# Performance work log

Measured on AMD Instinct MI355X. Metric: run time of the kernel, lower is better.

The kernel has to match this reference:

```python
import jax, jax.numpy as jnp
import numpy as np

N_NODES = 100000
N_EDGES = 1600000
N_GRAPHS = 64
IN_F = 128
H_F = 128
N_CLS = 10


def setup_inputs() -> dict:
    key = jax.random.key(0)
    ks = jax.random.split(key, 10)
    feat = jax.random.normal(ks[0], (N_NODES, IN_F), dtype=jnp.float32)
    W1 = jax.random.normal(ks[1], (IN_F, H_F), dtype=jnp.float32) * 0.05
    b1 = jax.random.normal(ks[2], (H_F,), dtype=jnp.float32) * 0.05
    W2 = jax.random.normal(ks[3], (H_F, H_F), dtype=jnp.float32) * 0.05
    b2 = jax.random.normal(ks[4], (H_F,), dtype=jnp.float32) * 0.05
    Wp = jax.random.normal(ks[5], (H_F, N_CLS), dtype=jnp.float32) * 0.05
    bp = jax.random.normal(ks[6], (N_CLS,), dtype=jnp.float32) * 0.05
    src = jax.random.randint(ks[7], (N_EDGES,), 0, N_NODES, dtype=jnp.int32)
    dst = jax.random.randint(ks[8], (N_EDGES,), 0, N_NODES, dtype=jnp.int32)
    graph_id = jnp.sort(jax.random.randint(ks[9], (N_NODES,), 0, N_GRAPHS, dtype=jnp.int32))
    return {"feat": feat, "W1": W1, "b1": b1, "W2": W2, "b2": b2,
            "Wp": Wp, "bp": bp, "src": src, "dst": dst, "graph_id": graph_id}


def reference(feat, W1, b1, W2, b2, Wp, bp, src, dst, graph_id):
    # copy_u + sum: each dst node sums features of its source neighbors
    def agg(h):
        return jax.ops.segment_sum(h[src], dst, num_segments=N_NODES)

    h = jax.nn.relu(agg(feat) @ W1 + b1)   # conv1 + ReLU
    h = jax.nn.relu(agg(h) @ W2 + b2)      # conv2 + ReLU (num_messagepasses=2)

    # dgl.mean_nodes: per-graph mean pooling over nodes
    sums = jax.ops.segment_sum(h, graph_id, num_segments=N_GRAPHS)      # [G, H]
    cnts = jax.ops.segment_sum(jnp.ones((N_NODES, 1), h.dtype), graph_id,
                               num_segments=N_GRAPHS)                    # [G, 1]
    graph_feats = sums / jnp.maximum(cnts, 1.0)
    return graph_feats @ Wp + bp
```

## Files before the change

kernel.cpp:

```cpp
#include <hip/hip_runtime.h>

#define NF 128
#define NGRAPHS 64
#define NCLS 10
#define NPARTS 256
#define PART_SHIFT 9
#define PART_NODES 512
#define PART_CAP 9216
#define SPLIT_TILE 4096
#define AS_STRIDE 136
#define SRC_BITS 17

typedef __attribute__((ext_vector_type(8))) short bf16x8;
typedef __attribute__((ext_vector_type(4))) float f32x4;
typedef __attribute__((ext_vector_type(8))) unsigned short u16x8;

__device__ __forceinline__ float bf2f(unsigned short u) {
    union { unsigned int i; float f; } v; v.i = ((unsigned int)u) << 16; return v.f;
}
__device__ __forceinline__ unsigned short f2bf(float f) {
    union { float f; unsigned int i; } v; v.f = f;
    unsigned int lsb = (v.i >> 16) & 1;
    v.i += 0x7fffu + lsb;
    return (unsigned short)(v.i >> 16);
}

__device__ __forceinline__ void gather_node(
    const unsigned short* __restrict__ x, const int* __restrict__ offs,
    const int* __restrict__ eid, int node, int n, int c, float acc[8]) {
#pragma unroll
    for (int r = 0; r < 8; ++r) acc[r] = 0.f;
    if (node >= n) return;
    int j = offs[node];
    int end = offs[node + 1];
    for (; j + 8 <= end; j += 8) {
        int s0 = eid[j + 0], s1 = eid[j + 1], s2 = eid[j + 2], s3 = eid[j + 3];
        int s4 = eid[j + 4], s5 = eid[j + 5], s6 = eid[j + 6], s7 = eid[j + 7];
        u16x8 v0 = ((const u16x8*)(x + (size_t)s0 * NF))[c];
        u16x8 v1 = ((const u16x8*)(x + (size_t)s1 * NF))[c];
        u16x8 v2 = ((const u16x8*)(x + (size_t)s2 * NF))[c];
        u16x8 v3 = ((const u16x8*)(x + (size_t)s3 * NF))[c];
        u16x8 v4 = ((const u16x8*)(x + (size_t)s4 * NF))[c];
        u16x8 v5 = ((const u16x8*)(x + (size_t)s5 * NF))[c];
        u16x8 v6 = ((const u16x8*)(x + (size_t)s6 * NF))[c];
        u16x8 v7 = ((const u16x8*)(x + (size_t)s7 * NF))[c];
#pragma unroll
        for (int r = 0; r < 8; ++r)
            acc[r] += ((bf2f(v0[r]) + bf2f(v1[r])) + (bf2f(v2[r]) + bf2f(v3[r])))
                    + ((bf2f(v4[r]) + bf2f(v5[r])) + (bf2f(v6[r]) + bf2f(v7[r])));
    }
    if (j + 4 <= end) {
        int s0 = eid[j + 0], s1 = eid[j + 1], s2 = eid[j + 2], s3 = eid[j + 3];
        u16x8 v0 = ((const u16x8*)(x + (size_t)s0 * NF))[c];
        u16x8 v1 = ((const u16x8*)(x + (size_t)s1 * NF))[c];
        u16x8 v2 = ((const u16x8*)(x + (size_t)s2 * NF))[c];
        u16x8 v3 = ((const u16x8*)(x + (size_t)s3 * NF))[c];
#pragma unroll
        for (int r = 0; r < 8; ++r)
            acc[r] += (bf2f(v0[r]) + bf2f(v1[r])) + (bf2f(v2[r]) + bf2f(v3[r]));
        j += 4;
    }
    for (; j < end; ++j) {
        int s0 = eid[j];
        u16x8 v0 = ((const u16x8*)(x + (size_t)s0 * NF))[c];
#pragma unroll
        for (int r = 0; r < 8; ++r) acc[r] += bf2f(v0[r]);
    }
}

__global__ __launch_bounds__(256) void split_prep_kernel(
    const int* __restrict__ src, const int* __restrict__ dst,
    unsigned int* __restrict__ records, int* __restrict__ gcur,
    const float* __restrict__ feat, unsigned short* __restrict__ featbf,
    const float* __restrict__ W1, const float* __restrict__ W2,
    unsigned short* __restrict__ Wt1, unsigned short* __restrict__ Wt2,
    float* __restrict__ sums, int ne, int nv4) {
    __shared__ unsigned int stage[SPLIT_TILE];
    __shared__ int hcnt[NPARTS];
    __shared__ int hscan[NPARTS];
    __shared__ int hcur[NPARTS];
    __shared__ int hg[NPARTS];
    int t = threadIdx.x;
    int gtid = blockIdx.x * 256 + t;
    int nthreads = gridDim.x * 256;

    for (int i = gtid; i < nv4; i += nthreads) {
        float4 v = ((const float4*)feat)[i];
        ushort4 o;
        o.x = f2bf(v.x); o.y = f2bf(v.y); o.z = f2bf(v.z); o.w = f2bf(v.w);
        ((ushort4*)featbf)[i] = o;
    }
    for (int i = gtid; i < 2 * NF * NF; i += nthreads) {
        const float* W = (i < NF * NF) ? W1 : W2;
        unsigned short* Wt = (i < NF * NF) ? Wt1 : Wt2;
        int id = i & (NF * NF - 1);
        int f = id >> 7;
        int k = id & 127;
        Wt[f * NF + k] = f2bf(W[k * NF + f]);
    }
    for (int i = gtid; i < NGRAPHS * NF; i += nthreads) sums[i] = 0.f;

    int tile0 = blockIdx.x * SPLIT_TILE;
    int cnt = min(SPLIT_TILE, ne - tile0);
    if (cnt <= 0) return;
    hcnt[t] = 0;
    __syncthreads();
    int dv[16], sv[16];
#pragma unroll
    for (int k2 = 0; k2 < 16; ++k2) {
        int i = k2 * 256 + t;
        if (i < cnt) {
            dv[k2] = dst[tile0 + i];
            sv[k2] = src[tile0 + i];
            atomicAdd(&hcnt[dv[k2] >> PART_SHIFT], 1);
        }
    }
    __syncthreads();
    hscan[t] = hcnt[t];
    __syncthreads();
    for (int off = 1; off < NPARTS; off <<= 1) {
        int v = (t >= off) ? hscan[t - off] : 0;
        __syncthreads();
        hscan[t] += v;
        __syncthreads();
    }
    hcur[t] = hscan[t] - hcnt[t];
    hg[t] = hcnt[t] ? atomicAdd(&gcur[t], hcnt[t]) : 0;
    __syncthreads();
#pragma unroll
    for (int k2 = 0; k2 < 16; ++k2) {
        int i = k2 * 256 + t;
        if (i < cnt) {
            int d = dv[k2];
            int pos = atomicAdd(&hcur[d >> PART_SHIFT], 1);
            stage[pos] = (((unsigned int)(d & (PART_NODES - 1))) << SRC_BITS)
                         | (unsigned int)sv[k2];
        }
    }
    __syncthreads();
    int grp = t >> 4;
    int lt = t & 15;
    for (int p = grp; p < NPARTS; p += 16) {
        int c = hcnt[p];
        if (c == 0) continue;
        int b = hscan[p] - c;
        int g = hg[p];
        if (g + c > PART_CAP) c = max(0, PART_CAP - g);
        unsigned int* outp = records + (size_t)p * PART_CAP + g;
        for (int i = lt; i < c; i += 16) outp[i] = stage[b + i];
    }
}

__global__ __launch_bounds__(256) void build_kernel(
    const unsigned int* __restrict__ records, const int* __restrict__ gcur,
    int* __restrict__ offs, int* __restrict__ eid, int n) {
    __shared__ int deg[PART_NODES];
    __shared__ int ps[NPARTS];
    __shared__ int wsum[4];
    __shared__ unsigned int rc[PART_CAP];
    int t = threadIdx.x;
    int p = blockIdx.x;

    ps[t] = min(gcur[t], PART_CAP);
    __syncthreads();
    for (int off = 1; off < NPARTS; off <<= 1) {
        int v = (t >= off) ? ps[t - off] : 0;
        __syncthreads();
        ps[t] += v;
        __syncthreads();
    }
    int L = min(gcur[p], PART_CAP);
    int base_g = ps[p] - L;
    if (p == 0 && t == 0) offs[n] = ps[NPARTS - 1];

    int lo = p << PART_SHIFT;
    int nn = min(n - lo, PART_NODES);
    if (nn <= 0) return;

    deg[t] = 0;
    deg[t + 256] = 0;
    __syncthreads();

    const unsigned int* rp = records + (size_t)p * PART_CAP;
    for (int i = t; i < L; i += 256) {
        unsigned int r = rp[i];
        rc[i] = r;
        atomicAdd(&deg[r >> SRC_BITS], 1);
    }
    __syncthreads();

    int v0 = deg[2 * t];
    int v1 = deg[2 * t + 1];
    int tsum = v0 + v1;
    int lane = t & 63, w = t >> 6;
    int sc = tsum;
    for (int off = 1; off < 64; off <<= 1) {
        int u = __shfl_up(sc, off, 64);
        if (lane >= off) sc += u;
    }
    if (lane == 63) wsum[w] = sc;
    __syncthreads();
    if (t == 0) {
        int a = 0;
        for (int k = 0; k < 4; ++k) { int v = wsum[k]; wsum[k] = a; a += v; }
    }
    __syncthreads();
    int run = sc - tsum + wsum[w];
    deg[2 * t] = run;
    if (2 * t < nn) offs[lo + 2 * t] = base_g + run;
    run += v0;
    deg[2 * t + 1] = run;
    if (2 * t + 1 < nn) offs[lo + 2 * t + 1] = base_g + run;
    __syncthreads();

    for (int i = t; i < L; i += 256) {
        unsigned int r = rc[i];
        int pos = atomicAdd(&deg[r >> SRC_BITS], 1);
        eid[base_g + pos] = (int)(r & ((1u << SRC_BITS) - 1));
    }
}

__global__ __launch_bounds__(256) void gather_gemm1(
    const unsigned short* __restrict__ x, const int* __restrict__ offs,
    const int* __restrict__ eid, const unsigned short* __restrict__ Wt,
    const float* __restrict__ bias, unsigned short* __restrict__ out, int n) {
    __shared__ unsigned short As[16 * AS_STRIDE];
    int wave = threadIdx.x >> 6;
    int lane = threadIdx.x & 63;
    int q = lane >> 4;
    int c = lane & 15;
    int node_base = blockIdx.x * 16;
    int row = wave * 4 + q;

    float acc[8];
    gather_node(x, offs, eid, node_base + row, n, c, acc);
    {
        u16x8 o;
#pragma unroll
        for (int r = 0; r < 8; ++r) o[r] = f2bf(acc[r]);
        *(u16x8*)(&As[row * AS_STRIDE + c * 8]) = o;
    }
    __syncthreads();

    int m16 = c;
    int n0 = wave * 32;
    const unsigned short* b0r = Wt + (size_t)(n0 + m16) * NF + q * 8;
    const unsigned short* b1r = b0r + 16 * NF;
    f32x4 acc0 = {0.f, 0.f, 0.f, 0.f};
    f32x4 acc1 = {0.f, 0.f, 0.f, 0.f};
#pragma unroll
    for (int kk = 0; kk < 4; ++kk) {
        bf16x8 a  = *(const bf16x8*)(&As[m16 * AS_STRIDE + kk * 32 + q * 8]);
        bf16x8 b0 = *(const bf16x8*)(b0r + kk * 32);
        bf16x8 b1 = *(const bf16x8*)(b1r + kk * 32);
        acc0 = __builtin_amdgcn_mfma_f32_16x16x32_bf16(a, b0, acc0, 0, 0, 0);
        acc1 = __builtin_amdgcn_mfma_f32_16x16x32_bf16(a, b1, acc1, 0, 0, 0);
    }
    float bias0 = bias[n0 + m16];
    float bias1 = bias[n0 + 16 + m16];
#pragma unroll
    for (int r = 0; r < 4; ++r) {
        int node = node_base + q * 4 + r;
        if (node >= n) break;
        unsigned short* o = out + (size_t)node * NF;
        o[n0 + m16]      = f2bf(fmaxf(acc0[r] + bias0, 0.f));
        o[n0 + 16 + m16] = f2bf(fmaxf(acc1[r] + bias1, 0.f));
    }
}

__global__ __launch_bounds__(256) void gather_gemm2_pool(
    const unsigned short* __restrict__ x, const int* __restrict__ offs,
    const int* __restrict__ eid, const unsigned short* __restrict__ Wt,
    const float* __restrict__ bias, const int* __restrict__ gid,
    float* __restrict__ sums, int n) {
    __shared__ unsigned short As[16 * AS_STRIDE];
    __shared__ float hblk[16][NF];
    int wave = threadIdx.x >> 6;
    int lane = threadIdx.x & 63;
    int q = lane >> 4;
    int c = lane & 15;
    int node_base = blockIdx.x * 16;
    int row = wave * 4 + q;

    float acc[8];
    gather_node(x, offs, eid, node_base + row, n, c, acc);
    {
        u16x8 o;
#pragma unroll
        for (int r = 0; r < 8; ++r) o[r] = f2bf(acc[r]);
        *(u16x8*)(&As[row * AS_STRIDE + c * 8]) = o;
    }
    __syncthreads();

    int m16 = c;
    int n0 = wave * 32;
    const unsigned short* b0r = Wt + (size_t)(n0 + m16) * NF + q * 8;
    const unsigned short* b1r = b0r + 16 * NF;
    f32x4 acc0 = {0.f, 0.f, 0.f, 0.f};
    f32x4 acc1 = {0.f, 0.f, 0.f, 0.f};
#pragma unroll
    for (int kk = 0; kk < 4; ++kk) {
        bf16x8 a  = *(const bf16x8*)(&As[m16 * AS_STRIDE + kk * 32 + q * 8]);
        bf16x8 b0 = *(const bf16x8*)(b0r + kk * 32);
        bf16x8 b1 = *(const bf16x8*)(b1r + kk * 32);
        acc0 = __builtin_amdgcn_mfma_f32_16x16x32_bf16(a, b0, acc0, 0, 0, 0);
        acc1 = __builtin_amdgcn_mfma_f32_16x16x32_bf16(a, b1, acc1, 0, 0, 0);
    }
    float bias0 = bias[n0 + m16];
    float bias1 = bias[n0 + 16 + m16];
#pragma unroll
    for (int r = 0; r < 4; ++r) {
        int rr = q * 4 + r;
        hblk[rr][n0 + m16]      = fmaxf(acc0[r] + bias0, 0.f);
        hblk[rr][n0 + 16 + m16] = fmaxf(acc1[r] + bias1, 0.f);
    }
    __syncthreads();

    int t = threadIdx.x;
    if (t < NF) {
        float accp = 0.f;
        int cur = -1;
        int lim = min(16, n - node_base);
        for (int i = 0; i < lim; ++i) {
            int g = gid[node_base + i];
            if (g != cur) {
                if (cur >= 0) atomicAdd(&sums[cur * NF + t], accp);
                accp = 0.f;
                cur = g;
            }
            accp += bf2f(f2bf(hblk[i][t]));
        }
        if (cur >= 0) atomicAdd(&sums[cur * NF + t], accp);
    }
}

__device__ __forceinline__ int lower_bound_i(const int* a, int n, int key) {
    int lo = 0, hi = n;
    while (lo < hi) {
        int mid = (lo + hi) >> 1;
        if (a[mid] < key) lo = mid + 1; else hi = mid;
    }
    return lo;
}

__global__ __launch_bounds__(64) void final_kernel(
    const float* __restrict__ sums, const int* __restrict__ gid, int n,
    const float* __restrict__ Wp, const float* __restrict__ bp,
    float* __restrict__ out) {
    __shared__ int range[2];
    int g = blockIdx.x;
    int c = threadIdx.x;
    if (c == 0) range[0] = lower_bound_i(gid, n, g);
    if (c == 1) range[1] = lower_bound_i(gid, n, g + 1);
    __syncthreads();
    if (c >= NCLS) return;
    float cnt = fmaxf((float)(range[1] - range[0]), 1.0f);
    float inv = 1.0f / cnt;
    float acc = bp[c];
#pragma unroll 8
    for (int k = 0; k < NF; ++k) {
        acc += sums[g * NF + k] * inv * Wp[k * NCLS + c];
    }
    out[g * NCLS + c] = acc;
}

extern "C" void kernel_launch(void* const* d_in, const int* in_sizes, int n_in,
                              void* d_out, int out_size, void* d_ws, size_t ws_size,
                              hipStream_t stream) {
    const float* feat = (const float*)d_in[0];
    const float* W1   = (const float*)d_in[1];
    const float* b1   = (const float*)d_in[2];
    const float* W2   = (const float*)d_in[3];
    const float* b2   = (const float*)d_in[4];
    const float* Wp   = (const float*)d_in[5];
    const float* bp   = (const float*)d_in[6];
    const int*   src  = (const int*)d_in[7];
    const int*   dst  = (const int*)d_in[8];
    const int*   gid  = (const int*)d_in[9];

    int ne = in_sizes[7];
    int n  = in_sizes[9];

    unsigned short* featbf = (unsigned short*)d_ws;
    unsigned short* h1     = featbf + (size_t)n * NF;
    unsigned int* records = (unsigned int*)(h1 + (size_t)n * NF);
    int* eid      = (int*)(records + (size_t)NPARTS * PART_CAP);
    float* sums   = (float*)(eid + ne);
    int* gcur     = (int*)(sums + NGRAPHS * NF);
    unsigned short* Wt1 = (unsigned short*)(gcur + NPARTS);
    unsigned short* Wt2 = Wt1 + NF * NF;
    int* offs     = (int*)(Wt2 + NF * NF);

    int nv4 = n * NF / 4;
    int splitblocks = (ne + SPLIT_TILE - 1) / SPLIT_TILE;
    int buildblocks = (n + PART_NODES - 1) >> PART_SHIFT;
    int ggblocks = (n + 15) / 16;

    hipMemsetAsync(gcur, 0, NPARTS * sizeof(int), stream);
    split_prep_kernel<<<splitblocks, 256, 0, stream>>>(
        src, dst, records, gcur, feat, featbf, W1, W2, Wt1, Wt2, sums, ne, nv4);
    build_kernel<<<buildblocks, 256, 0, stream>>>(records, gcur, offs, eid, n);

    gather_gemm1<<<ggblocks, 256, 0, stream>>>(featbf, offs, eid, Wt1, b1, h1, n);
    gather_gemm2_pool<<<ggblocks, 256, 0, stream>>>(h1, offs, eid, Wt2, b2, gid, sums, n);
    final_kernel<<<NGRAPHS, 64, 0, stream>>>(sums, gid, n, Wp, bp, (float*)d_out);
}
```

Baseline: 306.8 us.

## Slice features into 16-column planes and split gather from GEMM kernels

```diff
diff --git a/kernel.cpp b/kernel.cpp
--- a/kernel.cpp
+++ b/kernel.cpp
@@ -11,6 +11,10 @@
 #define AS_STRIDE 136
 #define SRC_BITS 17
 
+#define NSLICE 8
+#define SL 16
+#define AGG_TILE 32
+
 typedef __attribute__((ext_vector_type(8))) short bf16x8;
 typedef __attribute__((ext_vector_type(4))) float f32x4;
 typedef __attribute__((ext_vector_type(8))) unsigned short u16x8;
@@ -23,49 +27,6 @@
     unsigned int lsb = (v.i >> 16) & 1;
     v.i += 0x7fffu + lsb;
     return (unsigned short)(v.i >> 16);
-}
-
-__device__ __forceinline__ void gather_node(
-    const unsigned short* __restrict__ x, const int* __restrict__ offs,
-    const int* __restrict__ eid, int node, int n, int c, float acc[8]) {
-#pragma unroll
-    for (int r = 0; r < 8; ++r) acc[r] = 0.f;
-    if (node >= n) return;
-    int j = offs[node];
-    int end = offs[node + 1];
-    for (; j + 8 <= end; j += 8) {
-        int s0 = eid[j + 0], s1 = eid[j + 1], s2 = eid[j + 2], s3 = eid[j + 3];
-        int s4 = eid[j + 4], s5 = eid[j + 5], s6 = eid[j + 6], s7 = eid[j + 7];
-        u16x8 v0 = ((const u16x8*)(x + (size_t)s0 * NF))[c];
-        u16x8 v1 = ((const u16x8*)(x + (size_t)s1 * NF))[c];
-        u16x8 v2 = ((const u16x8*)(x + (size_t)s2 * NF))[c];
-        u16x8 v3 = ((const u16x8*)(x + (size_t)s3 * NF))[c];
-        u16x8 v4 = ((const u16x8*)(x + (size_t)s4 * NF))[c];
-        u16x8 v5 = ((const u16x8*)(x + (size_t)s5 * NF))[c];
-        u16x8 v6 = ((const u16x8*)(x + (size_t)s6 * NF))[c];
-        u16x8 v7 = ((const u16x8*)(x + (size_t)s7 * NF))[c];
-#pragma unroll
-        for (int r = 0; r < 8; ++r)
-            acc[r] += ((bf2f(v0[r]) + bf2f(v1[r])) + (bf2f(v2[r]) + bf2f(v3[r])))
-                    + ((bf2f(v4[r]) + bf2f(v5[r])) + (bf2f(v6[r]) + bf2f(v7[r])));
-    }
-    if (j + 4 <= end) {
-        int s0 = eid[j + 0], s1 = eid[j + 1], s2 = eid[j + 2], s3 = eid[j + 3];
-        u16x8 v0 = ((const u16x8*)(x + (size_t)s0 * NF))[c];
-        u16x8 v1 = ((const u16x8*)(x + (size_t)s1 * NF))[c];
-        u16x8 v2 = ((const u16x8*)(x + (size_t)s2 * NF))[c];
-        u16x8 v3 = ((const u16x8*)(x + (size_t)s3 * NF))[c];
-#pragma unroll
-        for (int r = 0; r < 8; ++r)
-            acc[r] += (bf2f(v0[r]) + bf2f(v1[r])) + (bf2f(v2[r]) + bf2f(v3[r]));
-        j += 4;
-    }
-    for (; j < end; ++j) {
-        int s0 = eid[j];
-        u16x8 v0 = ((const u16x8*)(x + (size_t)s0 * NF))[c];
-#pragma unroll
-        for (int r = 0; r < 8; ++r) acc[r] += bf2f(v0[r]);
-    }
 }
 
 __global__ __launch_bounds__(256) void split_prep_kernel(
@@ -83,12 +44,17 @@
     int t = threadIdx.x;
     int gtid = blockIdx.x * 256 + t;
     int nthreads = gridDim.x * 256;
+    int n_nodes = nv4 >> 5;
 
     for (int i = gtid; i < nv4; i += nthreads) {
         float4 v = ((const float4*)feat)[i];
         ushort4 o;
         o.x = f2bf(v.x); o.y = f2bf(v.y); o.z = f2bf(v.z); o.w = f2bf(v.w);
-        ((ushort4*)featbf)[i] = o;
+        int node = i >> 5;
+        int q4 = i & 31;
+        int s = q4 >> 2;
+        int cc = (q4 & 3) * 4;
+        *(ushort4*)(featbf + ((size_t)s * n_nodes + node) * SL + cc) = o;
     }
     for (int i = gtid; i < 2 * NF * NF; i += nthreads) {
         const float* W = (i < NF * NF) ? W1 : W2;
@@ -220,29 +186,86 @@
     }
 }
 
-__global__ __launch_bounds__(256) void gather_gemm1(
-    const unsigned short* __restrict__ x, const int* __restrict__ offs,
-    const int* __restrict__ eid, const unsigned short* __restrict__ Wt,
-    const float* __restrict__ bias, unsigned short* __restrict__ out, int n) {
+__global__ __launch_bounds__(256) void agg_slice(
+    const unsigned short* __restrict__ xs,
+    const int* __restrict__ offs, const int* __restrict__ eid,
+    unsigned short* __restrict__ out,
+    int n) {
+    __shared__ unsigned short ob[AGG_TILE * SL];
+    int b = blockIdx.x;
+    int s = b & 7;
+    int node0 = (b >> 3) * AGG_TILE;
+    const unsigned short* xb = xs + (size_t)s * n * SL;
+    int t = threadIdx.x;
+    int wave = t >> 6;
+    int lane = t & 63;
+    int hw = lane >> 5;
+    int l = lane & 31;
+    int slot = l >> 1;
+    int half = l & 1;
+
+#pragma unroll
+    for (int r = 0; r < AGG_TILE / 8; ++r) {
+        int node = node0 + r * 8 + wave * 2 + hw;
+        float acc[8] = {0.f, 0.f, 0.f, 0.f, 0.f, 0.f, 0.f, 0.f};
+        if (node < n) {
+            int beg = __builtin_nontemporal_load(offs + node);
+            int end = __builtin_nontemporal_load(offs + node + 1);
+            for (int j = beg + slot; j < end; j += 16) {
+                int srcv = __builtin_nontemporal_load(eid + j);
+                u16x8 v = *(const u16x8*)(xb + (size_t)srcv * SL + half * 8);
+#pragma unroll
+                for (int k = 0; k < 8; ++k) acc[k] += bf2f(v[k]);
+            }
+        }
+#pragma unroll
+        for (int m = 2; m <= 16; m <<= 1) {
+#pragma unroll
+            for (int k = 0; k < 8; ++k) acc[k] += __shfl_xor(acc[k], m, 64);
+        }
+        if (slot == 0) {
+            u16x8 o;
+#pragma unroll
+            for (int k = 0; k < 8; ++k) o[k] = f2bf(acc[k]);
+            *(u16x8*)(&ob[(r * 8 + wave * 2 + hw) * SL + half * 8]) = o;
+        }
+    }
+    __syncthreads();
+    int nrem = n - node0;
+    if (nrem > AGG_TILE) nrem = AGG_TILE;
+    if (nrem > 0) {
+        int cu16 = nrem * SL;
+        int i = t * 2;
+        if (i < cu16) {
+            unsigned int w = *(const unsigned int*)(&ob[i]);
+            *(unsigned int*)(out + ((size_t)s * n + node0) * SL + i) = w;
+        }
+    }
+}
+
+__global__ __launch_bounds__(256) void gemm_h1(
+    unsigned short* __restrict__ buf,
+    const unsigned short* __restrict__ Wt, const float* __restrict__ bias,
+    int n) {
     __shared__ unsigned short As[16 * AS_STRIDE];
-    int wave = threadIdx.x >> 6;
-    int lane = threadIdx.x & 63;
+    int t = threadIdx.x;
+    int node_base = blockIdx.x * 16;
+    {
+        int s = t >> 5;
+        int u = t & 31;
+        int r = u >> 1;
+        int hc = (u & 1) * 8;
+        int node = node_base + r;
+        u16x8 v = {0, 0, 0, 0, 0, 0, 0, 0};
+        if (node < n) v = *(const u16x8*)(buf + ((size_t)s * n + node) * SL + hc);
+        *(u16x8*)(&As[r * AS_STRIDE + s * SL + hc]) = v;
+    }
+    __syncthreads();
+
+    int wave = t >> 6;
+    int lane = t & 63;
     int q = lane >> 4;
-    int c = lane & 15;
-    int node_base = blockIdx.x * 16;
-    int row = wave * 4 + q;
-
-    float acc[8];
-    gather_node(x, offs, eid, node_base + row, n, c, acc);
-    {
-        u16x8 o;
-#pragma unroll
-        for (int r = 0; r < 8; ++r) o[r] = f2bf(acc[r]);
-        *(u16x8*)(&As[row * AS_STRIDE + c * 8]) = o;
-    }
-    __syncthreads();
-
-    int m16 = c;
+    int m16 = lane & 15;
     int n0 = wave * 32;
     const unsigned short* b0r = Wt + (size_t)(n0 + m16) * NF + q * 8;
     const unsigned short* b1r = b0r + 16 * NF;
@@ -262,37 +285,37 @@
     for (int r = 0; r < 4; ++r) {
         int node = node_base + q * 4 + r;
         if (node >= n) break;
-        unsigned short* o = out + (size_t)node * NF;
-        o[n0 + m16]      = f2bf(fmaxf(acc0[r] + bias0, 0.f));
-        o[n0 + 16 + m16] = f2bf(fmaxf(acc1[r] + bias1, 0.f));
-    }
-}
-
-__global__ __launch_bounds__(256) void gather_gemm2_pool(
-    const unsigned short* __restrict__ x, const int* __restrict__ offs,
-    const int* __restrict__ eid, const unsigned short* __restrict__ Wt,
-    const float* __restrict__ bias, const int* __restrict__ gid,
-    float* __restrict__ sums, int n) {
+        buf[((size_t)(2 * wave) * n + node) * SL + m16] =
+            f2bf(fmaxf(acc0[r] + bias0, 0.f));
+        buf[((size_t)(2 * wave + 1) * n + node) * SL + m16] =
+            f2bf(fmaxf(acc1[r] + bias1, 0.f));
+    }
+}
+
+__global__ __launch_bounds__(256) void gemm_h2_pool(
+    const unsigned short* __restrict__ buf,
+    const unsigned short* __restrict__ Wt, const float* __restrict__ bias,
+    const int* __restrict__ gid, float* __restrict__ sums, int n) {
     __shared__ unsigned short As[16 * AS_STRIDE];
     __shared__ float hblk[16][NF];
-    int wave = threadIdx.x >> 6;
-    int lane = threadIdx.x & 63;
+    int t = threadIdx.x;
+    int node_base = blockIdx.x * 16;
+    {
+        int s = t >> 5;
+        int u = t & 31;
+        int r = u >> 1;
+        int hc = (u & 1) * 8;
+        int node = node_base + r;
+        u16x8 v = {0, 0, 0, 0, 0, 0, 0, 0};
+        if (node < n) v = *(const u16x8*)(buf + ((size_t)s * n + node) * SL + hc);
+        *(u16x8*)(&As[r * AS_STRIDE + s * SL + hc]) = v;
+    }
+    __syncthreads();
+
+    int wave = t >> 6;
+    int lane = t & 63;
     int q = lane >> 4;
-    int c = lane & 15;
-    int node_base = blockIdx.x * 16;
-    int row = wave * 4 + q;
-
-    float acc[8];
-    gather_node(x, offs, eid, node_base + row, n, c, acc);
-    {
-        u16x8 o;
-#pragma unroll
-        for (int r = 0; r < 8; ++r) o[r] = f2bf(acc[r]);
-        *(u16x8*)(&As[row * AS_STRIDE + c * 8]) = o;
-    }
-    __syncthreads();
-
-    int m16 = c;
+    int m16 = lane & 15;
     int n0 = wave * 32;
     const unsigned short* b0r = Wt + (size_t)(n0 + m16) * NF + q * 8;
     const unsigned short* b1r = b0r + 16 * NF;
@@ -310,13 +333,12 @@
     float bias1 = bias[n0 + 16 + m16];
 #pragma unroll
     for (int r = 0; r < 4; ++r) {
-        int rr = q * 4 + r;
-        hblk[rr][n0 + m16]      = fmaxf(acc0[r] + bias0, 0.f);
-        hblk[rr][n0 + 16 + m16] = fmaxf(acc1[r] + bias1, 0.f);
-    }
-    __syncthreads();
-
-    int t = threadIdx.x;
+        int row = q * 4 + r;
+        hblk[row][n0 + m16]      = fmaxf(acc0[r] + bias0, 0.f);
+        hblk[row][n0 + 16 + m16] = fmaxf(acc1[r] + bias1, 0.f);
+    }
+    __syncthreads();
+
     if (t < NF) {
         float accp = 0.f;
         int cur = -1;
@@ -381,9 +403,9 @@
     int ne = in_sizes[7];
     int n  = in_sizes[9];
 
-    unsigned short* featbf = (unsigned short*)d_ws;
-    unsigned short* h1     = featbf + (size_t)n * NF;
-    unsigned int* records = (unsigned int*)(h1 + (size_t)n * NF);
+    unsigned short* bufA = (unsigned short*)d_ws;
+    unsigned short* bufB = bufA + (size_t)n * NF;
+    unsigned int* records = (unsigned int*)(bufB + (size_t)n * NF);
     int* eid      = (int*)(records + (size_t)NPARTS * PART_CAP);
     float* sums   = (float*)(eid + ne);
     int* gcur     = (int*)(sums + NGRAPHS * NF);
@@ -394,14 +416,17 @@
     int nv4 = n * NF / 4;
     int splitblocks = (ne + SPLIT_TILE - 1) / SPLIT_TILE;
     int buildblocks = (n + PART_NODES - 1) >> PART_SHIFT;
-    int ggblocks = (n + 15) / 16;
+    int aggblocks = NSLICE * ((n + AGG_TILE - 1) / AGG_TILE);
+    int gemmblocks = (n + 15) / 16;
 
     hipMemsetAsync(gcur, 0, NPARTS * sizeof(int), stream);
     split_prep_kernel<<<splitblocks, 256, 0, stream>>>(
-        src, dst, records, gcur, feat, featbf, W1, W2, Wt1, Wt2, sums, ne, nv4);
+        src, dst, records, gcur, feat, bufA, W1, W2, Wt1, Wt2, sums, ne, nv4);
     build_kernel<<<buildblocks, 256, 0, stream>>>(records, gcur, offs, eid, n);
 
-    gather_gemm1<<<ggblocks, 256, 0, stream>>>(featbf, offs, eid, Wt1, b1, h1, n);
-    gather_gemm2_pool<<<ggblocks, 256, 0, stream>>>(h1, offs, eid, Wt2, b2, gid, sums, n);
+    agg_slice<<<aggblocks, 256, 0, stream>>>(bufA, offs, eid, bufB, n);
+    gemm_h1<<<gemmblocks, 256, 0, stream>>>(bufB, Wt1, b1, n);
+    agg_slice<<<aggblocks, 256, 0, stream>>>(bufB, offs, eid, bufA, n);
+    gemm_h2_pool<<<gemmblocks, 256, 0, stream>>>(bufA, Wt2, b2, gid, sums, n);
     final_kernel<<<NGRAPHS, 64, 0, stream>>>(sums, gid, n, Wp, bp, (float*)d_out);
 }
```

New measurement: 538.7 us. 1.76x slower.

## Stage neighbor rows into LDS via global_load_lds in gather_gemm1

Applied to the files above, without the earlier changes.

```diff
diff --git a/kernel.cpp b/kernel.cpp
--- a/kernel.cpp
+++ b/kernel.cpp
@@ -23,6 +23,13 @@
     unsigned int lsb = (v.i >> 16) & 1;
     v.i += 0x7fffu + lsb;
     return (unsigned short)(v.i >> 16);
+}
+
+__device__ __forceinline__ void load_lds16(const unsigned short* g,
+                                           unsigned short* l) {
+    __builtin_amdgcn_global_load_lds(
+        (const __attribute__((address_space(1))) void*)g,
+        (__attribute__((address_space(3))) void*)l, 16, 0, 0);
 }
 
 __device__ __forceinline__ void gather_node(
@@ -225,24 +232,46 @@
     const int* __restrict__ eid, const unsigned short* __restrict__ Wt,
     const float* __restrict__ bias, unsigned short* __restrict__ out, int n) {
     __shared__ unsigned short As[16 * AS_STRIDE];
+    __shared__ unsigned short stg[4][16][NF];
     int wave = threadIdx.x >> 6;
     int lane = threadIdx.x & 63;
+    int node_base = blockIdx.x * 16;
+    unsigned short* myst = &stg[wave][0][0];
+
+    for (int i = 0; i < 4; ++i) {
+        int row = wave * 4 + i;
+        int node = node_base + row;
+        float a0 = 0.f, a1 = 0.f;
+        if (node < n) {
+            int beg = offs[node];
+            int end = offs[node + 1];
+            for (int j0 = beg; j0 < end; j0 += 16) {
+                asm volatile("s_waitcnt lgkmcnt(0)" ::: "memory");
+                int cnt = end - j0;
+                if (cnt > 16) cnt = 16;
+                int nch = (cnt + 3) >> 2;
+                for (int ch = 0; ch < nch; ++ch) {
+                    int sj = j0 + ch * 4 + (lane >> 4);
+                    int e = eid[sj < end ? sj : beg];
+                    const unsigned short* gp = x + (size_t)e * NF + (lane & 15) * 8;
+                    load_lds16(gp, myst + ch * 512);
+                }
+                asm volatile("s_waitcnt vmcnt(0)" ::: "memory");
+                for (int s = 0; s < cnt; ++s) {
+                    unsigned int w = *(const unsigned int*)(myst + s * NF + lane * 2);
+                    a0 += bf2f((unsigned short)(w & 0xffffu));
+                    a1 += bf2f((unsigned short)(w >> 16));
+                }
+                asm volatile("" ::: "memory");
+            }
+        }
+        *(unsigned int*)(&As[row * AS_STRIDE + lane * 2]) =
+            ((unsigned int)f2bf(a1) << 16) | (unsigned int)f2bf(a0);
+    }
+    __syncthreads();
+
     int q = lane >> 4;
-    int c = lane & 15;
-    int node_base = blockIdx.x * 16;
-    int row = wave * 4 + q;
-
-    float acc[8];
-    gather_node(x, offs, eid, node_base + row, n, c, acc);
-    {
-        u16x8 o;
-#pragma unroll
-        for (int r = 0; r < 8; ++r) o[r] = f2bf(acc[r]);
-        *(u16x8*)(&As[row * AS_STRIDE + c * 8]) = o;
-    }
-    __syncthreads();
-
-    int m16 = c;
+    int m16 = lane & 15;
     int n0 = wave * 32;
     const unsigned short* b0r = Wt + (size_t)(n0 + m16) * NF + q * 8;
     const unsigned short* b1r = b0r + 16 * NF;
```

Measured after the change: 315.8 us. 2.9% more time.

## Split prep and partition kernels, halve split tile, parallelize final projection

Applied to the files above, without the earlier changes.

```diff
diff --git a/kernel.cpp b/kernel.cpp
--- a/kernel.cpp
+++ b/kernel.cpp
@@ -7,7 +7,7 @@
 #define PART_SHIFT 9
 #define PART_NODES 512
 #define PART_CAP 9216
-#define SPLIT_TILE 4096
+#define SPLIT_TILE 2048
 #define AS_STRIDE 136
 #define SRC_BITS 17
 
@@ -68,22 +68,13 @@
     }
 }
 
-__global__ __launch_bounds__(256) void split_prep_kernel(
-    const int* __restrict__ src, const int* __restrict__ dst,
-    unsigned int* __restrict__ records, int* __restrict__ gcur,
+__global__ __launch_bounds__(256) void prep_kernel(
     const float* __restrict__ feat, unsigned short* __restrict__ featbf,
     const float* __restrict__ W1, const float* __restrict__ W2,
     unsigned short* __restrict__ Wt1, unsigned short* __restrict__ Wt2,
-    float* __restrict__ sums, int ne, int nv4) {
-    __shared__ unsigned int stage[SPLIT_TILE];
-    __shared__ int hcnt[NPARTS];
-    __shared__ int hscan[NPARTS];
-    __shared__ int hcur[NPARTS];
-    __shared__ int hg[NPARTS];
-    int t = threadIdx.x;
-    int gtid = blockIdx.x * 256 + t;
+    float* __restrict__ sums, int* __restrict__ gcur, int nv4) {
+    int gtid = blockIdx.x * 256 + threadIdx.x;
     int nthreads = gridDim.x * 256;
-
     for (int i = gtid; i < nv4; i += nthreads) {
         float4 v = ((const float4*)feat)[i];
         ushort4 o;
@@ -99,15 +90,27 @@
         Wt[f * NF + k] = f2bf(W[k * NF + f]);
     }
     for (int i = gtid; i < NGRAPHS * NF; i += nthreads) sums[i] = 0.f;
+    if (gtid < NPARTS) gcur[gtid] = 0;
+}
+
+__global__ __launch_bounds__(256) void split_kernel(
+    const int* __restrict__ src, const int* __restrict__ dst,
+    unsigned int* __restrict__ records, int* __restrict__ gcur, int ne) {
+    __shared__ unsigned int stage[SPLIT_TILE];
+    __shared__ int hcnt[NPARTS];
+    __shared__ int hscan[NPARTS];
+    __shared__ int hcur[NPARTS];
+    __shared__ int hg[NPARTS];
+    int t = threadIdx.x;
 
     int tile0 = blockIdx.x * SPLIT_TILE;
     int cnt = min(SPLIT_TILE, ne - tile0);
     if (cnt <= 0) return;
     hcnt[t] = 0;
     __syncthreads();
-    int dv[16], sv[16];
-#pragma unroll
-    for (int k2 = 0; k2 < 16; ++k2) {
+    int dv[SPLIT_TILE / 256], sv[SPLIT_TILE / 256];
+#pragma unroll
+    for (int k2 = 0; k2 < SPLIT_TILE / 256; ++k2) {
         int i = k2 * 256 + t;
         if (i < cnt) {
             dv[k2] = dst[tile0 + i];
@@ -128,7 +131,7 @@
     hg[t] = hcnt[t] ? atomicAdd(&gcur[t], hcnt[t]) : 0;
     __syncthreads();
 #pragma unroll
-    for (int k2 = 0; k2 < 16; ++k2) {
+    for (int k2 = 0; k2 < SPLIT_TILE / 256; ++k2) {
         int i = k2 * 256 + t;
         if (i < cnt) {
             int d = dv[k2];
@@ -349,19 +352,21 @@
     float* __restrict__ out) {
     __shared__ int range[2];
     int g = blockIdx.x;
-    int c = threadIdx.x;
-    if (c == 0) range[0] = lower_bound_i(gid, n, g);
-    if (c == 1) range[1] = lower_bound_i(gid, n, g + 1);
-    __syncthreads();
-    if (c >= NCLS) return;
+    int lane = threadIdx.x;
+    if (lane == 0) range[0] = lower_bound_i(gid, n, g);
+    if (lane == 1) range[1] = lower_bound_i(gid, n, g + 1);
+    __syncthreads();
     float cnt = fmaxf((float)(range[1] - range[0]), 1.0f);
     float inv = 1.0f / cnt;
-    float acc = bp[c];
-#pragma unroll 8
-    for (int k = 0; k < NF; ++k) {
-        acc += sums[g * NF + k] * inv * Wp[k * NCLS + c];
-    }
-    out[g * NCLS + c] = acc;
+    float s0 = sums[g * NF + lane] * inv;
+    float s1 = sums[g * NF + 64 + lane] * inv;
+#pragma unroll
+    for (int c = 0; c < NCLS; ++c) {
+        float p = s0 * Wp[lane * NCLS + c] + s1 * Wp[(64 + lane) * NCLS + c];
+#pragma unroll
+        for (int m = 1; m < 64; m <<= 1) p += __shfl_xor(p, m, 64);
+        if (lane == 0) out[g * NCLS + c] = p + bp[c];
+    }
 }
 
 extern "C" void kernel_launch(void* const* d_in, const int* in_sizes, int n_in,
@@ -396,9 +401,9 @@
     int buildblocks = (n + PART_NODES - 1) >> PART_SHIFT;
     int ggblocks = (n + 15) / 16;
 
-    hipMemsetAsync(gcur, 0, NPARTS * sizeof(int), stream);
-    split_prep_kernel<<<splitblocks, 256, 0, stream>>>(
-        src, dst, records, gcur, feat, featbf, W1, W2, Wt1, Wt2, sums, ne, nv4);
+    prep_kernel<<<1024, 256, 0, stream>>>(
+        feat, featbf, W1, W2, Wt1, Wt2, sums, gcur, nv4);
+    split_kernel<<<splitblocks, 256, 0, stream>>>(src, dst, records, gcur, ne);
     build_kernel<<<buildblocks, 256, 0, stream>>>(records, gcur, offs, eid, n);
 
     gather_gemm1<<<ggblocks, 256, 0, stream>>>(featbf, offs, eid, Wt1, b1, h1, n);
```

Result: no change. 309.6 us (+0.9%).
